# Optimization experiments

Hardware: AMD Instinct MI355X
Metric: run time of the kernel (lower is better)

Reference implementation:

```python
import jax, jax.numpy as jnp
import numpy as np

N_NODES = 100_000
N_EDGES = 1_600_000  # avg degree 16
D_FEAT = 64


def setup_inputs() -> dict:
    key = jax.random.key(0)
    k_x, k_val, k_src, k_dst = jax.random.split(key, 4)
    x = jax.random.normal(k_x, (N_NODES, D_FEAT), dtype=jnp.float32)
    edge_val = jax.random.uniform(k_val, (N_EDGES,), dtype=jnp.float32)
    edge_src = jax.random.randint(k_src, (N_EDGES,), 0, N_NODES, dtype=jnp.int32)
    edge_dst = jax.random.randint(k_dst, (N_EDGES,), 0, N_NODES, dtype=jnp.int32)
    return {"x": x, "edge_val": edge_val, "edge_src": edge_src, "edge_dst": edge_dst}


def reference(x, edge_val, edge_src, edge_dst):
    # out = adj @ x  with adj in COO form:
    # out[dst] += val * x[src]   (sparse-dense matmul, SpMM)
    msgs = x[edge_src] * edge_val[:, None]          # [E, D] gather + scale
    out = jax.ops.segment_sum(msgs, edge_dst, num_segments=N_NODES)  # [N, D] scatter-add
    return out
```

## Files before the change

### kernel.cpp

```cpp
#include <hip/hip_runtime.h>

#define N_NODES 100000
#define N_EDGES 1600000
#define D_FEAT 64
#define NPB 128
#define K_BUCKETS 782
#define CAP 2304
#define A_BLOCKS 400
#define A_CHUNK 4000

__global__ void scatterA(const int* __restrict__ src, const int* __restrict__ dst,
                         const float* __restrict__ val, int* __restrict__ cursor,
                         int2* __restrict__ bdata) {
    __shared__ int sh_cnt[K_BUCKETS];
    __shared__ int sh_base[K_BUCKETS];
    for (int i = threadIdx.x; i < K_BUCKETS; i += 256) sh_cnt[i] = 0;
    __syncthreads();
    const int base = blockIdx.x * A_CHUNK;
    for (int j = threadIdx.x; j < A_CHUNK; j += 256)
        atomicAdd(&sh_cnt[dst[base + j] >> 7], 1);
    __syncthreads();
    for (int i = threadIdx.x; i < K_BUCKETS; i += 256) {
        const int c = sh_cnt[i];
        sh_base[i] = c ? (i * CAP + atomicAdd(&cursor[i], c)) : 0;
    }
    __syncthreads();
    for (int i = threadIdx.x; i < K_BUCKETS; i += 256) sh_cnt[i] = 0;
    __syncthreads();
    for (int j = threadIdx.x; j < A_CHUNK; j += 256) {
        const int e = base + j;
        const int d = dst[e];
        const int b = d >> 7;
        const int slot = atomicAdd(&sh_cnt[b], 1);
        bdata[sh_base[b] + slot] =
            make_int2(src[e] | ((d & 127) << 17), __float_as_int(val[e]));
    }
}

__global__ void sortB(int2* __restrict__ bdata, const int* __restrict__ cursor,
                      int* __restrict__ rbeg, int* __restrict__ rdeg) {
    __shared__ int2 sh_e[CAP];
    __shared__ int cnt[NPB];
    __shared__ int cur[NPB];
    const int b = blockIdx.x;
    const int count = min(cursor[b], CAP);
    const int base = b * CAP;
    const int t = threadIdx.x;
    if (t < NPB) cnt[t] = 0;
    __syncthreads();
    for (int j = t; j < count; j += 256) {
        const int2 e = bdata[base + j];
        sh_e[j] = e;
        atomicAdd(&cnt[e.x >> 17], 1);
    }
    __syncthreads();
    const int v = (t < NPB) ? cnt[t] : 0;
    for (int off = 1; off < NPB; off <<= 1) {
        int u = 0;
        if (t < NPB && t >= off) u = cnt[t - off];
        __syncthreads();
        if (t < NPB) cnt[t] += u;
        __syncthreads();
    }
    const int row0 = b * NPB;
    if (t < NPB) {
        const int excl = cnt[t] - v;
        cur[t] = excl;
        if (row0 + t < N_NODES) { rbeg[row0 + t] = base + excl; rdeg[row0 + t] = v; }
    }
    __syncthreads();
    for (int j = t; j < count; j += 256) {
        const int2 pv = sh_e[j];
        const int dl = pv.x >> 17;
        const int slot = atomicAdd(&cur[dl], 1);
        bdata[base + slot] = make_int2(pv.x & 0x1FFFF, pv.y);
    }
}

__global__ void spmm_csr(const float* __restrict__ x,
                         const int* __restrict__ rbeg,
                         const int* __restrict__ rdeg,
                         const int2* __restrict__ csr,
                         float* __restrict__ out) {
    const int tid = blockIdx.x * blockDim.x + threadIdx.x;
    const int row = tid >> 4;
    const int c = tid & 15;
    if (row >= N_NODES) return;
    const int beg = rbeg[row];
    const int end = beg + rdeg[row];
    float4 acc = {0.f, 0.f, 0.f, 0.f};
    int j = beg;
    for (; j + 2 <= end; j += 2) {
        const int2 p0 = csr[j];
        const int2 p1 = csr[j + 1];
        const float4 m0 = ((const float4*)(x + (size_t)p0.x * D_FEAT))[c];
        const float4 m1 = ((const float4*)(x + (size_t)p1.x * D_FEAT))[c];
        const float v0 = __int_as_float(p0.y);
        const float v1 = __int_as_float(p1.y);
        acc.x += v0 * m0.x + v1 * m1.x;
        acc.y += v0 * m0.y + v1 * m1.y;
        acc.z += v0 * m0.z + v1 * m1.z;
        acc.w += v0 * m0.w + v1 * m1.w;
    }
    if (j < end) {
        const int2 p0 = csr[j];
        const float4 m0 = ((const float4*)(x + (size_t)p0.x * D_FEAT))[c];
        const float v0 = __int_as_float(p0.y);
        acc.x += v0 * m0.x;
        acc.y += v0 * m0.y;
        acc.z += v0 * m0.z;
        acc.w += v0 * m0.w;
    }
    ((float4*)(out + (size_t)row * D_FEAT))[c] = acc;
}

extern "C" void kernel_launch(void* const* d_in, const int* in_sizes, int n_in,
                              void* d_out, int out_size, void* d_ws, size_t ws_size,
                              hipStream_t stream) {
    const float* x        = (const float*)d_in[0];
    const float* edge_val = (const float*)d_in[1];
    const int*   edge_src = (const int*)d_in[2];
    const int*   edge_dst = (const int*)d_in[3];
    float* out = (float*)d_out;

    int* ws     = (int*)d_ws;
    int* cursor = ws;
    int* rbeg   = cursor + K_BUCKETS;
    int* rdeg   = rbeg + N_NODES;
    size_t used = (size_t)K_BUCKETS + 2 * N_NODES;
    used = (used + 1) & ~(size_t)1;
    int2* bdata = (int2*)(ws + used);

    hipMemsetAsync(cursor, 0, K_BUCKETS * sizeof(int), stream);

    const int B = 256;
    const int gridRow = (N_NODES * 16 + B - 1) / B;

    scatterA<<<A_BLOCKS, 256, 0, stream>>>(edge_src, edge_dst, edge_val, cursor, bdata);
    sortB   <<<K_BUCKETS, 256, 0, stream>>>(bdata, cursor, rbeg, rdeg);
    spmm_csr<<<gridRow, B, 0, stream>>>(x, rbeg, rdeg, bdata, out);
}
```

Measured before the change: 191.5 us.

## Stage bucketed edges in LDS for coalesced writes; unroll SpMM gather by four

The scatter kernel now uses an in-block prefix sum to sort each chunk's edges by bucket in shared memory, then writes them to the global bucket array in order, so consecutive threads store to contiguous addresses instead of scattered ones. This uses about 48KB of LDS per block, which may lower occupancy. The SpMM kernel unrolls its edge loop from two to four, putting more independent x-row gathers in flight per thread, and handles the remainder with a scalar loop.

```diff
diff --git a/kernel.cpp b/kernel.cpp
--- a/kernel.cpp
+++ b/kernel.cpp
@@ -9,32 +9,63 @@
 #define A_BLOCKS 400
 #define A_CHUNK 4000
 
-__global__ void scatterA(const int* __restrict__ src, const int* __restrict__ dst,
-                         const float* __restrict__ val, int* __restrict__ cursor,
-                         int2* __restrict__ bdata) {
-    __shared__ int sh_cnt[K_BUCKETS];
-    __shared__ int sh_base[K_BUCKETS];
-    for (int i = threadIdx.x; i < K_BUCKETS; i += 256) sh_cnt[i] = 0;
+__global__ __launch_bounds__(256)
+void scatterA(const int* __restrict__ src, const int* __restrict__ dst,
+              const float* __restrict__ val, int* __restrict__ cursor,
+              int2* __restrict__ bdata) {
+    __shared__ int  sh_cnt[K_BUCKETS];
+    __shared__ int  sh_off[K_BUCKETS];
+    __shared__ int  sh_gb[K_BUCKETS];
+    __shared__ int  sh_tsum[256];
+    __shared__ int2 sh_e[A_CHUNK];
+    __shared__ int  sh_ga[A_CHUNK];
+    const int t = threadIdx.x;
+    for (int i = t; i < K_BUCKETS; i += 256) sh_cnt[i] = 0;
     __syncthreads();
     const int base = blockIdx.x * A_CHUNK;
-    for (int j = threadIdx.x; j < A_CHUNK; j += 256)
+    for (int j = t; j < A_CHUNK; j += 256)
         atomicAdd(&sh_cnt[dst[base + j] >> 7], 1);
     __syncthreads();
-    for (int i = threadIdx.x; i < K_BUCKETS; i += 256) {
-        const int c = sh_cnt[i];
-        sh_base[i] = c ? (i * CAP + atomicAdd(&cursor[i], c)) : 0;
+    {
+        const int idx = 4 * t;
+        const int a0 = (idx + 0 < K_BUCKETS) ? sh_cnt[idx + 0] : 0;
+        const int a1 = (idx + 1 < K_BUCKETS) ? sh_cnt[idx + 1] : 0;
+        const int a2 = (idx + 2 < K_BUCKETS) ? sh_cnt[idx + 2] : 0;
+        const int a3 = (idx + 3 < K_BUCKETS) ? sh_cnt[idx + 3] : 0;
+        const int s = a0 + a1 + a2 + a3;
+        sh_tsum[t] = s;
+        __syncthreads();
+        for (int off = 1; off < 256; off <<= 1) {
+            const int u = (t >= off) ? sh_tsum[t - off] : 0;
+            __syncthreads();
+            sh_tsum[t] += u;
+            __syncthreads();
+        }
+        const int excl = sh_tsum[t] - s;
+        if (idx + 0 < K_BUCKETS) sh_off[idx + 0] = excl;
+        if (idx + 1 < K_BUCKETS) sh_off[idx + 1] = excl + a0;
+        if (idx + 2 < K_BUCKETS) sh_off[idx + 2] = excl + a0 + a1;
+        if (idx + 3 < K_BUCKETS) sh_off[idx + 3] = excl + a0 + a1 + a2;
     }
     __syncthreads();
-    for (int i = threadIdx.x; i < K_BUCKETS; i += 256) sh_cnt[i] = 0;
+    for (int i = t; i < K_BUCKETS; i += 256) {
+        const int c = sh_cnt[i];
+        int gb = 0;
+        if (c) gb = i * CAP + atomicAdd(&cursor[i], c);
+        sh_gb[i] = gb - sh_off[i];
+    }
     __syncthreads();
-    for (int j = threadIdx.x; j < A_CHUNK; j += 256) {
+    for (int j = t; j < A_CHUNK; j += 256) {
         const int e = base + j;
         const int d = dst[e];
         const int b = d >> 7;
-        const int slot = atomicAdd(&sh_cnt[b], 1);
-        bdata[sh_base[b] + slot] =
-            make_int2(src[e] | ((d & 127) << 17), __float_as_int(val[e]));
+        const int pos = atomicAdd(&sh_off[b], 1);
+        sh_e[pos] = make_int2(src[e] | ((d & 127) << 17), __float_as_int(val[e]));
+        sh_ga[pos] = sh_gb[b] + pos;
     }
+    __syncthreads();
+    for (int j = t; j < A_CHUNK; j += 256)
+        bdata[sh_ga[j]] = sh_e[j];
 }
 
 __global__ void sortB(int2* __restrict__ bdata, const int* __restrict__ cursor,
@@ -87,22 +118,30 @@
     const int c = tid & 15;
     if (row >= N_NODES) return;
     const int beg = rbeg[row];
-    const int end = beg + rdeg[row];
+    const int deg = rdeg[row];
+    const int end = beg + deg;
     float4 acc = {0.f, 0.f, 0.f, 0.f};
     int j = beg;
-    for (; j + 2 <= end; j += 2) {
+    const int end4 = beg + (deg & ~3);
+    for (; j < end4; j += 4) {
         const int2 p0 = csr[j];
         const int2 p1 = csr[j + 1];
+        const int2 p2 = csr[j + 2];
+        const int2 p3 = csr[j + 3];
         const float4 m0 = ((const float4*)(x + (size_t)p0.x * D_FEAT))[c];
         const float4 m1 = ((const float4*)(x + (size_t)p1.x * D_FEAT))[c];
+        const float4 m2 = ((const float4*)(x + (size_t)p2.x * D_FEAT))[c];
+        const float4 m3 = ((const float4*)(x + (size_t)p3.x * D_FEAT))[c];
         const float v0 = __int_as_float(p0.y);
         const float v1 = __int_as_float(p1.y);
-        acc.x += v0 * m0.x + v1 * m1.x;
-        acc.y += v0 * m0.y + v1 * m1.y;
-        acc.z += v0 * m0.z + v1 * m1.z;
-        acc.w += v0 * m0.w + v1 * m1.w;
+        const float v2 = __int_as_float(p2.y);
+        const float v3 = __int_as_float(p3.y);
+        acc.x += v0 * m0.x + v1 * m1.x + v2 * m2.x + v3 * m3.x;
+        acc.y += v0 * m0.y + v1 * m1.y + v2 * m2.y + v3 * m3.y;
+        acc.z += v0 * m0.z + v1 * m1.z + v2 * m2.z + v3 * m3.z;
+        acc.w += v0 * m0.w + v1 * m1.w + v2 * m2.w + v3 * m3.w;
     }
-    if (j < end) {
+    for (; j < end; ++j) {
         const int2 p0 = csr[j];
         const float4 m0 = ((const float4*)(x + (size_t)p0.x * D_FEAT))[c];
         const float v0 = __int_as_float(p0.y);
```

Measured after the change: 193.3 us. No clear change (+1.0%).
